# Performance work log

Hardware: AMD Instinct MI355X
Metric: run time of the kernel (lower is better)

## Reference

```python
import jax, jax.numpy as jnp
import numpy as np

N, E, F_IN, H, C = 20000, 320000, 256, 4, 64
D = H * C  # hidden_dim = 256
NEG_SLOPE = 0.2
LN_EPS = 1e-5


def setup_inputs() -> dict:
    key = jax.random.key(0)
    ks = jax.random.split(key, 12)
    x = jax.random.normal(ks[0], (N, F_IN), dtype=jnp.float32)
    # edges guaranteed self-loop-free (PyG GATConv removes then re-adds self loops)
    dst = jax.random.randint(ks[1], (E,), 0, N)
    off = jax.random.randint(ks[2], (E,), 1, N)
    src = (dst + off) % N
    edge_index = jnp.stack([src, dst]).astype(jnp.int64)

    def lin(k, fan_in, shape):
        return jax.random.normal(k, shape, dtype=jnp.float32) / np.sqrt(fan_in)

    W1 = lin(ks[3], F_IN, (F_IN, D)); b1 = jnp.zeros((D,), jnp.float32)
    a_src1 = lin(ks[4], C, (H, C)); a_dst1 = lin(ks[5], C, (H, C))
    W2 = lin(ks[6], D, (D, D)); b2 = jnp.zeros((D,), jnp.float32)
    a_src2 = lin(ks[7], C, (H, C)); a_dst2 = lin(ks[8], C, (H, C))
    g1 = jnp.ones((D,), jnp.float32); be1 = jnp.zeros((D,), jnp.float32)
    g2 = jnp.ones((D,), jnp.float32); be2 = jnp.zeros((D,), jnp.float32)
    attn_w = lin(ks[9], D, (D, 1)); attn_b = jnp.zeros((1,), jnp.float32)
    return dict(x=x, edge_index=edge_index, W1=W1, b1=b1, a_src1=a_src1,
                a_dst1=a_dst1, W2=W2, b2=b2, a_src2=a_src2, a_dst2=a_dst2,
                g1=g1, be1=be1, g2=g2, be2=be2, attn_w=attn_w, attn_b=attn_b)


def _gat_conv(x, src, dst, W, b, a_src, a_dst):
    # x: [N, F] -> h: [N, H, C]
    h = (x @ W).reshape(N, H, C)
    alpha_s = jnp.einsum('nhc,hc->nh', h, a_src)  # [N, H]
    alpha_d = jnp.einsum('nhc,hc->nh', h, a_dst)
    e = jax.nn.leaky_relu(alpha_s[src] + alpha_d[dst], NEG_SLOPE)  # [E', H]
    # segment softmax over edges sharing a destination
    m = jax.ops.segment_max(e, dst, num_segments=N)
    w = jnp.exp(e - m[dst])
    z = jax.ops.segment_sum(w, dst, num_segments=N)
    alpha = w / (z[dst] + 1e-16)
    out = jax.ops.segment_sum(h[src] * alpha[:, :, None], dst, num_segments=N)
    return out.reshape(N, D) + b


def _layernorm(x, g, b):
    mu = x.mean(-1, keepdims=True)
    var = ((x - mu) ** 2).mean(-1, keepdims=True)
    return (x - mu) * jax.lax.rsqrt(var + LN_EPS) * g + b


def reference(x, edge_index, W1, b1, a_src1, a_dst1, W2, b2, a_src2, a_dst2,
              g1, be1, g2, be2, attn_w, attn_b):
    loops = jnp.arange(N, dtype=edge_index.dtype)
    src = jnp.concatenate([edge_index[0], loops])
    dst = jnp.concatenate([edge_index[1], loops])
    x1 = _gat_conv(x, src, dst, W1, b1, a_src1, a_dst1)
    x1 = jax.nn.elu(_layernorm(x1, g1, be1))
    x2 = _gat_conv(x1, src, dst, W2, b2, a_src2, a_dst2)
    x2 = jax.nn.elu(_layernorm(x2, g2, be2) + x1)
    attn = jax.nn.softmax(x2 @ attn_w + attn_b, axis=0)  # softmax over nodes
    pooled = (x2 * attn).sum(axis=0)  # [D]
    return pooled
```

## Files before the change

### kernel.cpp

```cpp
#include <hip/hip_runtime.h>
#include <math.h>

#define N_NODES 20000
#define E_EDGES 320000
#define TOT_E   (E_EDGES + N_NODES)
#define DHID    256
#define NHEAD   4
#define SCAN_NB ((N_NODES + 255) / 256)
#define SPART   32
#define ECAP    128

typedef float f32x4 __attribute__((ext_vector_type(4)));
typedef short short8 __attribute__((ext_vector_type(8)));
typedef unsigned short ushort;

__device__ __forceinline__ float wave_sum(float v) {
#pragma unroll
  for (int off = 32; off; off >>= 1) v += __shfl_xor(v, off);
  return v;
}
__device__ __forceinline__ ushort f2bf(float f) {
  unsigned u = __float_as_uint(f);
  u += 0x7fffu + ((u >> 16) & 1u);
  return (ushort)(u >> 16);
}
__device__ __forceinline__ float bflo(unsigned u) {
  return __uint_as_float(u << 16);
}
__device__ __forceinline__ float bfhi(unsigned u) {
  return __uint_as_float(u & 0xffff0000u);
}

__global__ void hist_kernel(const int* __restrict__ ei, int* __restrict__ deg) {
  int e = blockIdx.x * blockDim.x + threadIdx.x;
  if (e >= TOT_E) return;
  int dst = (e < E_EDGES) ? ei[E_EDGES + e] : (e - E_EDGES);
  atomicAdd(&deg[dst], 1);
}

__global__ __launch_bounds__(256)
void scan_blocks_kernel(const int* __restrict__ deg, int* __restrict__ bsum) {
  __shared__ int ws[4];
  const int t = threadIdx.x;
  const int i = blockIdx.x * 256 + t;
  int v = (i < N_NODES) ? deg[i] : 0;
  int s = v;
#pragma unroll
  for (int off = 32; off; off >>= 1) s += __shfl_xor(s, off);
  if ((t & 63) == 0) ws[t >> 6] = s;
  __syncthreads();
  if (t == 0) bsum[blockIdx.x] = ws[0] + ws[1] + ws[2] + ws[3];
}

__global__ __launch_bounds__(128)
void scan_tops_kernel(const int* __restrict__ bsum, int* __restrict__ boff) {
  __shared__ int tmp[SCAN_NB];
  const int t = threadIdx.x;
  if (t < SCAN_NB) tmp[t] = bsum[t];
  __syncthreads();
  if (t == 0) {
    int run = 0;
    for (int i = 0; i < SCAN_NB; ++i) { int x = tmp[i]; tmp[i] = run; run += x; }
  }
  __syncthreads();
  if (t < SCAN_NB) boff[t] = tmp[t];
}

__global__ __launch_bounds__(256)
void scan_apply_kernel(const int* __restrict__ deg, const int* __restrict__ boff,
                       int* __restrict__ rowp, int* __restrict__ cur) {
  __shared__ int ws[4];
  const int t = threadIdx.x;
  const int lane = t & 63, w = t >> 6;
  const int i = blockIdx.x * 256 + t;
  int v = (i < N_NODES) ? deg[i] : 0;
  int inc = v;
#pragma unroll
  for (int off = 1; off < 64; off <<= 1) {
    int u = __shfl_up(inc, off);
    if (lane >= off) inc += u;
  }
  if (lane == 63) ws[w] = inc;
  __syncthreads();
  int add = boff[blockIdx.x];
#pragma unroll
  for (int k = 0; k < 4; ++k)
    if (k < w) add += ws[k];
  int exc = add + inc - v;
  if (i < N_NODES) {
    rowp[i] = exc;
    cur[i] = exc;
    if (i == N_NODES - 1) rowp[N_NODES] = exc + v;
  }
}

__global__ void scatter_kernel(const int* __restrict__ ei, int* __restrict__ cur,
                               int* __restrict__ colb) {
  int e = blockIdx.x * blockDim.x + threadIdx.x;
  if (e >= TOT_E) return;
  int src, dst;
  if (e < E_EDGES) { src = ei[e]; dst = ei[E_EDGES + e]; }
  else             { src = dst = e - E_EDGES; }
  int pos = atomicAdd(&cur[dst], 1);
  colb[pos] = src;
}

__global__ __launch_bounds__(256)
void conv_inputs_kernel(const float* __restrict__ W1, const float* __restrict__ W2,
                        const float* __restrict__ x, ushort* __restrict__ Wt1,
                        ushort* __restrict__ Wt2, ushort* __restrict__ xb,
                        int* __restrict__ deg) {
  const int b = blockIdx.x;
  if (b < 512) {
    const float* W = (b < 256) ? W1 : W2;
    ushort* Wt = (b < 256) ? Wt1 : Wt2;
    const int n = b & 255;
    const int k = threadIdx.x;
    Wt[n * 256 + k] = f2bf(W[k * 256 + n]);
  } else if (b < 512 + N_NODES * 256 / 8 / 256) {
    int idx = (b - 512) * 256 + threadIdx.x;
    size_t base = (size_t)idx * 8;
    float4 a = *reinterpret_cast<const float4*>(x + base);
    float4 c = *reinterpret_cast<const float4*>(x + base + 4);
    short8 o;
    o[0] = f2bf(a.x); o[1] = f2bf(a.y); o[2] = f2bf(a.z); o[3] = f2bf(a.w);
    o[4] = f2bf(c.x); o[5] = f2bf(c.y); o[6] = f2bf(c.z); o[7] = f2bf(c.w);
    *reinterpret_cast<short8*>(xb + base) = o;
  } else {
    int idx = (b - (512 + N_NODES * 256 / 8 / 256)) * 256 + threadIdx.x;
    if (idx < N_NODES) deg[idx] = 0;
  }
}

__global__ __launch_bounds__(256)
void gemm_alpha_kernel(const ushort* __restrict__ Ab, const ushort* __restrict__ Wt,
                       const float* __restrict__ asrc, const float* __restrict__ adst,
                       ushort* __restrict__ hout, float* __restrict__ as_,
                       float* __restrict__ ad_) {
  __shared__ ushort hs[32 * 256];

  const int t = threadIdx.x;
  const int w = t >> 6;
  const int l = t & 63;
  const int row0 = blockIdx.x * 32;

  const ushort* abase = Ab + (size_t)(row0 + (l & 15)) * 256 + ((l >> 4) * 8);
  const ushort* bbase = Wt + (size_t)(w * 64 + (l & 15)) * 256 + ((l >> 4) * 8);

  f32x4 acc[2][4];
#pragma unroll
  for (int i = 0; i < 2; ++i)
#pragma unroll
    for (int j = 0; j < 4; ++j) acc[i][j] = (f32x4){0.f, 0.f, 0.f, 0.f};

  short8 a0 = *reinterpret_cast<const short8*>(abase);
  short8 a1 = *reinterpret_cast<const short8*>(abase + 16 * 256);
  short8 b0 = *reinterpret_cast<const short8*>(bbase);
  short8 b1 = *reinterpret_cast<const short8*>(bbase + 16 * 256);
  short8 b2 = *reinterpret_cast<const short8*>(bbase + 32 * 256);
  short8 b3 = *reinterpret_cast<const short8*>(bbase + 48 * 256);
#pragma unroll
  for (int kk = 0; kk < 256; kk += 32) {
    short8 na0, na1, nb0, nb1, nb2, nb3;
    if (kk + 32 < 256) {
      na0 = *reinterpret_cast<const short8*>(abase + kk + 32);
      na1 = *reinterpret_cast<const short8*>(abase + 16 * 256 + kk + 32);
      nb0 = *reinterpret_cast<const short8*>(bbase + kk + 32);
      nb1 = *reinterpret_cast<const short8*>(bbase + 16 * 256 + kk + 32);
      nb2 = *reinterpret_cast<const short8*>(bbase + 32 * 256 + kk + 32);
      nb3 = *reinterpret_cast<const short8*>(bbase + 48 * 256 + kk + 32);
    }
    acc[0][0] = __builtin_amdgcn_mfma_f32_16x16x32_bf16(a0, b0, acc[0][0], 0, 0, 0);
    acc[0][1] = __builtin_amdgcn_mfma_f32_16x16x32_bf16(a0, b1, acc[0][1], 0, 0, 0);
    acc[0][2] = __builtin_amdgcn_mfma_f32_16x16x32_bf16(a0, b2, acc[0][2], 0, 0, 0);
    acc[0][3] = __builtin_amdgcn_mfma_f32_16x16x32_bf16(a0, b3, acc[0][3], 0, 0, 0);
    acc[1][0] = __builtin_amdgcn_mfma_f32_16x16x32_bf16(a1, b0, acc[1][0], 0, 0, 0);
    acc[1][1] = __builtin_amdgcn_mfma_f32_16x16x32_bf16(a1, b1, acc[1][1], 0, 0, 0);
    acc[1][2] = __builtin_amdgcn_mfma_f32_16x16x32_bf16(a1, b2, acc[1][2], 0, 0, 0);
    acc[1][3] = __builtin_amdgcn_mfma_f32_16x16x32_bf16(a1, b3, acc[1][3], 0, 0, 0);
    if (kk + 32 < 256) {
      a0 = na0; a1 = na1; b0 = nb0; b1 = nb1; b2 = nb2; b3 = nb3;
    }
  }

  float asj[4], adj[4];
#pragma unroll
  for (int j = 0; j < 4; ++j) {
    asj[j] = asrc[w * 64 + j * 16 + (l & 15)];
    adj[j] = adst[w * 64 + j * 16 + (l & 15)];
  }
#pragma unroll
  for (int i = 0; i < 2; ++i) {
#pragma unroll
    for (int q = 0; q < 4; ++q) {
      float ps = 0.f, pd = 0.f;
#pragma unroll
      for (int j = 0; j < 4; ++j) {
        ps += acc[i][j][q] * asj[j];
        pd += acc[i][j][q] * adj[j];
      }
#pragma unroll
      for (int off = 1; off < 16; off <<= 1) {
        ps += __shfl_xor(ps, off);
        pd += __shfl_xor(pd, off);
      }
      int row = row0 + i * 16 + (l >> 4) * 4 + q;
      if ((l & 15) == 0) {
        as_[row * 4 + w] = ps;
        ad_[row * 4 + w] = pd;
      }
    }
  }

#pragma unroll
  for (int i = 0; i < 2; ++i)
#pragma unroll
    for (int j = 0; j < 4; ++j)
#pragma unroll
      for (int q = 0; q < 4; ++q) {
        int row = i * 16 + (l >> 4) * 4 + q;
        int col = w * 64 + j * 16 + (l & 15);
        hs[row * 256 + col] = f2bf(acc[i][j][q]);
      }
  __syncthreads();
#pragma unroll
  for (int g = 0; g < 4; ++g) {
    int gi = g * 256 + t;
    int row = gi >> 5;
    int slot = gi & 31;
    *reinterpret_cast<short8*>(hout + (size_t)(row0 + row) * 256 + slot * 8) =
        *reinterpret_cast<const short8*>(&hs[row * 256 + slot * 8]);
  }
}

__global__ __launch_bounds__(256)
void attn_gather_ln_kernel(const ushort* __restrict__ h, const float* __restrict__ as_,
                           const float* __restrict__ ad_, const int* __restrict__ rowp,
                           const int* __restrict__ colb, const float* __restrict__ bias,
                           const float* __restrict__ gamma, const float* __restrict__ beta,
                           const ushort* __restrict__ residb, ushort* __restrict__ outb,
                           const float* __restrict__ aw, const float* __restrict__ ab,
                           float* __restrict__ score) {
  __shared__ float ew[4][ECAP][NHEAD];
  __shared__ int   sidx[4][ECAP];

  const int t = threadIdx.x;
  const int wd = t >> 6;
  const int d = blockIdx.x * 4 + wd;
  const int l = t & 63;
  const int start = rowp[d];
  const int deg = rowp[d + 1] - start;
  const int* cb = colb + start;

  const int e16 = l >> 2, hh = l & 3;
  const float adv = ad_[d * 4 + hh];
  const int gh = l >> 4;
  const int c0 = l * 4;
  const ushort* hrow = h + c0;

  float zpart = 0.f;
  float a0 = 0.f, a1 = 0.f, a2 = 0.f, a3 = 0.f;

  for (int base = 0; base < deg; base += ECAP) {
    const int cnt = min(deg - base, ECAP);
    for (int i = e16; i < cnt; i += 16) {
      int s = cb[base + i];
      if (hh == 0) sidx[wd][i] = s;
      float e = as_[s * 4 + hh] + adv;
      e = (e >= 0.f) ? e : 0.2f * e;
      e = fminf(e, 60.f);
      float wv = __expf(e);
      ew[wd][i][hh] = wv;
      zpart += wv;
    }
    int i = 0;
    for (; i + 8 <= cnt; i += 8) {
      int ss[8]; float ww[8]; uint2 hv[8];
#pragma unroll
      for (int k = 0; k < 8; ++k) { ss[k] = sidx[wd][i + k]; ww[k] = ew[wd][i + k][gh]; }
#pragma unroll
      for (int k = 0; k < 8; ++k)
        hv[k] = *reinterpret_cast<const uint2*>(hrow + (size_t)ss[k] * 256);
#pragma unroll
      for (int k = 0; k < 8; ++k) {
        a0 += ww[k] * bflo(hv[k].x); a1 += ww[k] * bfhi(hv[k].x);
        a2 += ww[k] * bflo(hv[k].y); a3 += ww[k] * bfhi(hv[k].y);
      }
    }
    for (; i + 4 <= cnt; i += 4) {
      int ss[4]; float ww[4]; uint2 hv[4];
#pragma unroll
      for (int k = 0; k < 4; ++k) { ss[k] = sidx[wd][i + k]; ww[k] = ew[wd][i + k][gh]; }
#pragma unroll
      for (int k = 0; k < 4; ++k)
        hv[k] = *reinterpret_cast<const uint2*>(hrow + (size_t)ss[k] * 256);
#pragma unroll
      for (int k = 0; k < 4; ++k) {
        a0 += ww[k] * bflo(hv[k].x); a1 += ww[k] * bfhi(hv[k].x);
        a2 += ww[k] * bflo(hv[k].y); a3 += ww[k] * bfhi(hv[k].y);
      }
    }
    for (; i < cnt; ++i) {
      int s = sidx[wd][i];
      float wv = ew[wd][i][gh];
      uint2 hv = *reinterpret_cast<const uint2*>(hrow + (size_t)s * 256);
      a0 += wv * bflo(hv.x);
      a1 += wv * bfhi(hv.x);
      a2 += wv * bflo(hv.y);
      a3 += wv * bfhi(hv.y);
    }
  }

#pragma unroll
  for (int off = 4; off < 64; off <<= 1) zpart += __shfl_xor(zpart, off);
  const float zi = 1.f / (__shfl(zpart, gh) + 1e-16f);

  float4 bi = *reinterpret_cast<const float4*>(bias + c0);
  float v0 = a0 * zi + bi.x, v1 = a1 * zi + bi.y;
  float v2 = a2 * zi + bi.z, v3 = a3 * zi + bi.w;

  float s1 = wave_sum(v0 + v1 + v2 + v3);
  float s2 = wave_sum(v0 * v0 + v1 * v1 + v2 * v2 + v3 * v3);
  float mu = s1 * (1.f / 256.f);
  float var = s2 * (1.f / 256.f) - mu * mu;
  float rstd = rsqrtf(var + 1e-5f);
  float4 ga = *reinterpret_cast<const float4*>(gamma + c0);
  float4 be = *reinterpret_cast<const float4*>(beta + c0);
  float y0 = (v0 - mu) * rstd * ga.x + be.x;
  float y1 = (v1 - mu) * rstd * ga.y + be.y;
  float y2 = (v2 - mu) * rstd * ga.z + be.z;
  float y3 = (v3 - mu) * rstd * ga.w + be.w;
  if (residb) {
    uint2 rv = *reinterpret_cast<const uint2*>(residb + (size_t)d * 256 + c0);
    y0 += bflo(rv.x); y1 += bfhi(rv.x); y2 += bflo(rv.y); y3 += bfhi(rv.y);
  }
  y0 = (y0 > 0.f) ? y0 : expm1f(y0);
  y1 = (y1 > 0.f) ? y1 : expm1f(y1);
  y2 = (y2 > 0.f) ? y2 : expm1f(y2);
  y3 = (y3 > 0.f) ? y3 : expm1f(y3);

  uint2 o;
  o.x = ((unsigned)f2bf(y0)) | (((unsigned)f2bf(y1)) << 16);
  o.y = ((unsigned)f2bf(y2)) | (((unsigned)f2bf(y3)) << 16);
  *reinterpret_cast<uint2*>(outb + (size_t)d * 256 + c0) = o;

  if (score) {
    float4 aww = *reinterpret_cast<const float4*>(aw + c0);
    float sp = wave_sum(y0 * aww.x + y1 * aww.y + y2 * aww.z + y3 * aww.w);
    if (l == 0) score[d] = sp + ab[0];
  }
}

__global__ __launch_bounds__(256)
void score_part_kernel(const float* __restrict__ s, float* __restrict__ pm,
                       float* __restrict__ pz) {
  __shared__ float red[4];
  const int t = threadIdx.x, b = blockIdx.x;
  const int lane = t & 63, wid = t >> 6;
  float m = -INFINITY;
  for (int n = b * 256 + t; n < N_NODES; n += SPART * 256) m = fmaxf(m, s[n]);
#pragma unroll
  for (int off = 32; off; off >>= 1) m = fmaxf(m, __shfl_xor(m, off));
  if (lane == 0) red[wid] = m;
  __syncthreads();
  m = fmaxf(fmaxf(red[0], red[1]), fmaxf(red[2], red[3]));
  __syncthreads();
  float z = 0.f;
  for (int n = b * 256 + t; n < N_NODES; n += SPART * 256) z += __expf(s[n] - m);
  z = wave_sum(z);
  if (lane == 0) red[wid] = z;
  __syncthreads();
  if (t == 0) { pm[b] = m; pz[b] = red[0] + red[1] + red[2] + red[3]; }
}

__global__ __launch_bounds__(64)
void score_comb_kernel(const float* __restrict__ pm, const float* __restrict__ pz,
                       float* __restrict__ mz) {
  const int l = threadIdx.x;
  float m = (l < SPART) ? pm[l] : -INFINITY;
#pragma unroll
  for (int off = 32; off; off >>= 1) m = fmaxf(m, __shfl_xor(m, off));
  float z = (l < SPART) ? pz[l] * __expf(pm[l] - m) : 0.f;
  z = wave_sum(z);
  if (l == 0) { mz[0] = m; mz[1] = z; }
}

__global__ __launch_bounds__(256)
void pool_partial_kernel(const ushort* __restrict__ hb2, const float* __restrict__ s,
                         const float* __restrict__ mz, float* __restrict__ part) {
  __shared__ float red4[4][256];
  const int t = threadIdx.x, b = blockIdx.x;
  const int c4 = t & 63, rsub = t >> 6;
  const float m = mz[0];
  const float invz = 1.f / mz[1];
  f32x4 acc = (f32x4){0.f, 0.f, 0.f, 0.f};
  for (int n = b * 4 + rsub; n < N_NODES; n += 1024) {
    float w = __expf(s[n] - m);
    uint2 hv = *reinterpret_cast<const uint2*>(hb2 + (size_t)n * 256 + c4 * 4);
    acc[0] += w * bflo(hv.x);
    acc[1] += w * bfhi(hv.x);
    acc[2] += w * bflo(hv.y);
    acc[3] += w * bfhi(hv.y);
  }
#pragma unroll
  for (int k = 0; k < 4; ++k) red4[rsub][c4 * 4 + k] = acc[k];
  __syncthreads();
  if (t < 256) {
    float v = red4[0][t] + red4[1][t] + red4[2][t] + red4[3][t];
    part[b * 256 + t] = v * invz;
  }
}

__global__ __launch_bounds__(256)
void pool_final_kernel(const float* __restrict__ part, float* __restrict__ out) {
  const int t = threadIdx.x;
  float acc = 0.f;
  for (int b = 0; b < 256; ++b) acc += part[b * 256 + t];
  out[t] = acc;
}

extern "C" void kernel_launch(void* const* d_in, const int* in_sizes, int n_in,
                              void* d_out, int out_size, void* d_ws, size_t ws_size,
                              hipStream_t stream) {
  const float* x      = (const float*)d_in[0];
  const int*   ei     = (const int*)d_in[1];
  const float* W1     = (const float*)d_in[2];
  const float* b1     = (const float*)d_in[3];
  const float* a_src1 = (const float*)d_in[4];
  const float* a_dst1 = (const float*)d_in[5];
  const float* W2     = (const float*)d_in[6];
  const float* b2     = (const float*)d_in[7];
  const float* a_src2 = (const float*)d_in[8];
  const float* a_dst2 = (const float*)d_in[9];
  const float* g1     = (const float*)d_in[10];
  const float* be1    = (const float*)d_in[11];
  const float* g2     = (const float*)d_in[12];
  const float* be2    = (const float*)d_in[13];
  const float* attn_w = (const float*)d_in[14];
  const float* attn_b = (const float*)d_in[15];
  float* out = (float*)d_out;

  char* p = (char*)d_ws;
  auto alloc = [&](size_t bytes) {
    char* r = p;
    p += (bytes + 255) & ~size_t(255);
    return r;
  };
  ushort* h   = (ushort*)alloc((size_t)N_NODES * 256 * 2);
  ushort* xb  = (ushort*)alloc((size_t)N_NODES * 256 * 2);
  ushort* xb1 = (ushort*)alloc((size_t)N_NODES * 256 * 2);
  ushort* hb2 = (ushort*)alloc((size_t)N_NODES * 256 * 2);
  float* as_  = (float*)alloc((size_t)N_NODES * 4 * 4);
  float* ad_  = (float*)alloc((size_t)N_NODES * 4 * 4);
  float* sbuf = (float*)alloc((size_t)N_NODES * 4);
  float* mz   = (float*)alloc(256);
  float* pm   = (float*)alloc((size_t)SPART * 4);
  float* pz   = (float*)alloc((size_t)SPART * 4);
  float* part = (float*)alloc((size_t)256 * 256 * 4);
  ushort* wt1 = (ushort*)alloc((size_t)256 * 256 * 2);
  ushort* wt2 = (ushort*)alloc((size_t)256 * 256 * 2);
  int* deg    = (int*)alloc((size_t)N_NODES * 4);
  int* rowp   = (int*)alloc((size_t)(N_NODES + 1) * 4);
  int* cur    = (int*)alloc((size_t)N_NODES * 4);
  int* colb   = (int*)alloc((size_t)TOT_E * 4);
  int* bsum   = (int*)alloc((size_t)SCAN_NB * 4);
  int* boff   = (int*)alloc((size_t)SCAN_NB * 4);

  const int EB = (TOT_E + 255) / 256;
  const int GB = N_NODES / 32;
  const int DB = N_NODES / 4;
  const int XB = N_NODES * 256 / 8 / 256;
  const int CONVB = 512 + XB + SCAN_NB;

  conv_inputs_kernel<<<CONVB, 256, 0, stream>>>(W1, W2, x, wt1, wt2, xb, deg);
  hist_kernel<<<EB, 256, 0, stream>>>(ei, deg);
  scan_blocks_kernel<<<SCAN_NB, 256, 0, stream>>>(deg, bsum);
  scan_tops_kernel<<<1, 128, 0, stream>>>(bsum, boff);
  scan_apply_kernel<<<SCAN_NB, 256, 0, stream>>>(deg, boff, rowp, cur);
  scatter_kernel<<<EB, 256, 0, stream>>>(ei, cur, colb);

  gemm_alpha_kernel<<<GB, 256, 0, stream>>>(xb, wt1, a_src1, a_dst1, h, as_, ad_);
  attn_gather_ln_kernel<<<DB, 256, 0, stream>>>(h, as_, ad_, rowp, colb, b1, g1, be1,
                                                nullptr, xb1, nullptr, nullptr, nullptr);
  gemm_alpha_kernel<<<GB, 256, 0, stream>>>(xb1, wt2, a_src2, a_dst2, h, as_, ad_);
  attn_gather_ln_kernel<<<DB, 256, 0, stream>>>(h, as_, ad_, rowp, colb, b2, g2, be2,
                                                xb1, hb2, attn_w, attn_b, sbuf);
  score_part_kernel<<<SPART, 256, 0, stream>>>(sbuf, pm, pz);
  score_comb_kernel<<<1, 64, 0, stream>>>(pm, pz, mz);
  pool_partial_kernel<<<256, 256, 0, stream>>>(hb2, sbuf, mz, part);
  pool_final_kernel<<<1, 256, 0, stream>>>(part, out);
}
```

Baseline: 173.1 us.

## Cut launch count: single-block scan, merge scatter with GEMM, online-softmax pooling

Three launches for the degree prefix scan become one 1024-thread block that handles 20 elements per thread. The edge scatter and the first GEMM+alpha now run as a single launch with block-index dispatch, since neither depends on the other. The attention pooling uses an online softmax inside pool_partial, with the max and sum merged in pool_final, which removes the two score-reduction kernels. The aim is to reduce launch and serialization overhead, at the cost of a serial single-block scan and extra exp work in the pooling loop.

```diff
diff --git a/kernel.cpp b/kernel.cpp
--- a/kernel.cpp
+++ b/kernel.cpp
@@ -6,9 +6,9 @@
 #define TOT_E   (E_EDGES + N_NODES)
 #define DHID    256
 #define NHEAD   4
-#define SCAN_NB ((N_NODES + 255) / 256)
-#define SPART   32
 #define ECAP    128
+#define EB_K    ((TOT_E + 255) / 256)
+#define GB_K    (N_NODES / 32)
 
 typedef float f32x4 __attribute__((ext_vector_type(4)));
 typedef short short8 __attribute__((ext_vector_type(8)));
@@ -38,71 +38,45 @@
   atomicAdd(&deg[dst], 1);
 }
 
-__global__ __launch_bounds__(256)
-void scan_blocks_kernel(const int* __restrict__ deg, int* __restrict__ bsum) {
-  __shared__ int ws[4];
-  const int t = threadIdx.x;
-  const int i = blockIdx.x * 256 + t;
-  int v = (i < N_NODES) ? deg[i] : 0;
-  int s = v;
-#pragma unroll
-  for (int off = 32; off; off >>= 1) s += __shfl_xor(s, off);
-  if ((t & 63) == 0) ws[t >> 6] = s;
-  __syncthreads();
-  if (t == 0) bsum[blockIdx.x] = ws[0] + ws[1] + ws[2] + ws[3];
-}
-
-__global__ __launch_bounds__(128)
-void scan_tops_kernel(const int* __restrict__ bsum, int* __restrict__ boff) {
-  __shared__ int tmp[SCAN_NB];
-  const int t = threadIdx.x;
-  if (t < SCAN_NB) tmp[t] = bsum[t];
-  __syncthreads();
-  if (t == 0) {
-    int run = 0;
-    for (int i = 0; i < SCAN_NB; ++i) { int x = tmp[i]; tmp[i] = run; run += x; }
-  }
-  __syncthreads();
-  if (t < SCAN_NB) boff[t] = tmp[t];
-}
-
-__global__ __launch_bounds__(256)
-void scan_apply_kernel(const int* __restrict__ deg, const int* __restrict__ boff,
-                       int* __restrict__ rowp, int* __restrict__ cur) {
-  __shared__ int ws[4];
+__global__ __launch_bounds__(1024)
+void scan_kernel(const int* __restrict__ deg, int* __restrict__ rowp,
+                 int* __restrict__ cur) {
+  __shared__ int wsum[16];
   const int t = threadIdx.x;
   const int lane = t & 63, w = t >> 6;
-  const int i = blockIdx.x * 256 + t;
-  int v = (i < N_NODES) ? deg[i] : 0;
-  int inc = v;
+  const int base = t * 20;
+  int vals[20];
+  int sum = 0;
+#pragma unroll
+  for (int k = 0; k < 20; ++k) {
+    int i = base + k;
+    int v = (i < N_NODES) ? deg[i] : 0;
+    vals[k] = v;
+    sum += v;
+  }
+  int inc = sum;
 #pragma unroll
   for (int off = 1; off < 64; off <<= 1) {
     int u = __shfl_up(inc, off);
     if (lane >= off) inc += u;
   }
-  if (lane == 63) ws[w] = inc;
-  __syncthreads();
-  int add = boff[blockIdx.x];
-#pragma unroll
-  for (int k = 0; k < 4; ++k)
-    if (k < w) add += ws[k];
-  int exc = add + inc - v;
-  if (i < N_NODES) {
-    rowp[i] = exc;
-    cur[i] = exc;
-    if (i == N_NODES - 1) rowp[N_NODES] = exc + v;
-  }
-}
-
-__global__ void scatter_kernel(const int* __restrict__ ei, int* __restrict__ cur,
-                               int* __restrict__ colb) {
-  int e = blockIdx.x * blockDim.x + threadIdx.x;
-  if (e >= TOT_E) return;
-  int src, dst;
-  if (e < E_EDGES) { src = ei[e]; dst = ei[E_EDGES + e]; }
-  else             { src = dst = e - E_EDGES; }
-  int pos = atomicAdd(&cur[dst], 1);
-  colb[pos] = src;
+  if (lane == 63) wsum[w] = inc;
+  __syncthreads();
+  int add = 0;
+#pragma unroll
+  for (int k = 0; k < 16; ++k)
+    if (k < w) add += wsum[k];
+  int run = add + inc - sum;
+#pragma unroll
+  for (int k = 0; k < 20; ++k) {
+    int i = base + k;
+    if (i < N_NODES) {
+      rowp[i] = run;
+      cur[i] = run;
+      run += vals[k];
+    }
+  }
+  if (t == 0) rowp[N_NODES] = TOT_E;
 }
 
 __global__ __launch_bounds__(256)
@@ -133,6 +107,120 @@
 }
 
 __global__ __launch_bounds__(256)
+void scatter_gemm_kernel(const int* __restrict__ ei, int* __restrict__ cur,
+                         int* __restrict__ colb, const ushort* __restrict__ Ab,
+                         const ushort* __restrict__ Wt, const float* __restrict__ asrc,
+                         const float* __restrict__ adst, ushort* __restrict__ hout,
+                         float* __restrict__ as_, float* __restrict__ ad_) {
+  __shared__ ushort hs[32 * 256];
+
+  if (blockIdx.x < EB_K) {
+    int e = blockIdx.x * 256 + threadIdx.x;
+    if (e < TOT_E) {
+      int src, dst;
+      if (e < E_EDGES) { src = ei[e]; dst = ei[E_EDGES + e]; }
+      else             { src = dst = e - E_EDGES; }
+      int pos = atomicAdd(&cur[dst], 1);
+      colb[pos] = src;
+    }
+    return;
+  }
+
+  const int t = threadIdx.x;
+  const int w = t >> 6;
+  const int l = t & 63;
+  const int row0 = (blockIdx.x - EB_K) * 32;
+
+  const ushort* abase = Ab + (size_t)(row0 + (l & 15)) * 256 + ((l >> 4) * 8);
+  const ushort* bbase = Wt + (size_t)(w * 64 + (l & 15)) * 256 + ((l >> 4) * 8);
+
+  f32x4 acc[2][4];
+#pragma unroll
+  for (int i = 0; i < 2; ++i)
+#pragma unroll
+    for (int j = 0; j < 4; ++j) acc[i][j] = (f32x4){0.f, 0.f, 0.f, 0.f};
+
+  short8 a0 = *reinterpret_cast<const short8*>(abase);
+  short8 a1 = *reinterpret_cast<const short8*>(abase + 16 * 256);
+  short8 b0 = *reinterpret_cast<const short8*>(bbase);
+  short8 b1 = *reinterpret_cast<const short8*>(bbase + 16 * 256);
+  short8 b2 = *reinterpret_cast<const short8*>(bbase + 32 * 256);
+  short8 b3 = *reinterpret_cast<const short8*>(bbase + 48 * 256);
+#pragma unroll
+  for (int kk = 0; kk < 256; kk += 32) {
+    short8 na0, na1, nb0, nb1, nb2, nb3;
+    if (kk + 32 < 256) {
+      na0 = *reinterpret_cast<const short8*>(abase + kk + 32);
+      na1 = *reinterpret_cast<const short8*>(abase + 16 * 256 + kk + 32);
+      nb0 = *reinterpret_cast<const short8*>(bbase + kk + 32);
+      nb1 = *reinterpret_cast<const short8*>(bbase + 16 * 256 + kk + 32);
+      nb2 = *reinterpret_cast<const short8*>(bbase + 32 * 256 + kk + 32);
+      nb3 = *reinterpret_cast<const short8*>(bbase + 48 * 256 + kk + 32);
+    }
+    acc[0][0] = __builtin_amdgcn_mfma_f32_16x16x32_bf16(a0, b0, acc[0][0], 0, 0, 0);
+    acc[0][1] = __builtin_amdgcn_mfma_f32_16x16x32_bf16(a0, b1, acc[0][1], 0, 0, 0);
+    acc[0][2] = __builtin_amdgcn_mfma_f32_16x16x32_bf16(a0, b2, acc[0][2], 0, 0, 0);
+    acc[0][3] = __builtin_amdgcn_mfma_f32_16x16x32_bf16(a0, b3, acc[0][3], 0, 0, 0);
+    acc[1][0] = __builtin_amdgcn_mfma_f32_16x16x32_bf16(a1, b0, acc[1][0], 0, 0, 0);
+    acc[1][1] = __builtin_amdgcn_mfma_f32_16x16x32_bf16(a1, b1, acc[1][1], 0, 0, 0);
+    acc[1][2] = __builtin_amdgcn_mfma_f32_16x16x32_bf16(a1, b2, acc[1][2], 0, 0, 0);
+    acc[1][3] = __builtin_amdgcn_mfma_f32_16x16x32_bf16(a1, b3, acc[1][3], 0, 0, 0);
+    if (kk + 32 < 256) {
+      a0 = na0; a1 = na1; b0 = nb0; b1 = nb1; b2 = nb2; b3 = nb3;
+    }
+  }
+
+  float asj[4], adj[4];
+#pragma unroll
+  for (int j = 0; j < 4; ++j) {
+    asj[j] = asrc[w * 64 + j * 16 + (l & 15)];
+    adj[j] = adst[w * 64 + j * 16 + (l & 15)];
+  }
+#pragma unroll
+  for (int i = 0; i < 2; ++i) {
+#pragma unroll
+    for (int q = 0; q < 4; ++q) {
+      float ps = 0.f, pd = 0.f;
+#pragma unroll
+      for (int j = 0; j < 4; ++j) {
+        ps += acc[i][j][q] * asj[j];
+        pd += acc[i][j][q] * adj[j];
+      }
+#pragma unroll
+      for (int off = 1; off < 16; off <<= 1) {
+        ps += __shfl_xor(ps, off);
+        pd += __shfl_xor(pd, off);
+      }
+      int row = row0 + i * 16 + (l >> 4) * 4 + q;
+      if ((l & 15) == 0) {
+        as_[row * 4 + w] = ps;
+        ad_[row * 4 + w] = pd;
+      }
+    }
+  }
+
+#pragma unroll
+  for (int i = 0; i < 2; ++i)
+#pragma unroll
+    for (int j = 0; j < 4; ++j)
+#pragma unroll
+      for (int q = 0; q < 4; ++q) {
+        int row = i * 16 + (l >> 4) * 4 + q;
+        int col = w * 64 + j * 16 + (l & 15);
+        hs[row * 256 + col] = f2bf(acc[i][j][q]);
+      }
+  __syncthreads();
+#pragma unroll
+  for (int g = 0; g < 4; ++g) {
+    int gi = g * 256 + t;
+    int row = gi >> 5;
+    int slot = gi & 31;
+    *reinterpret_cast<short8*>(hout + (size_t)(row0 + row) * 256 + slot * 8) =
+        *reinterpret_cast<const short8*>(&hs[row * 256 + slot * 8]);
+  }
+}
+
+__global__ __launch_bounds__(256)
 void gemm_alpha_kernel(const ushort* __restrict__ Ab, const ushort* __restrict__ Wt,
                        const float* __restrict__ asrc, const float* __restrict__ adst,
                        ushort* __restrict__ hout, float* __restrict__ as_,
@@ -352,71 +440,67 @@
 }
 
 __global__ __launch_bounds__(256)
-void score_part_kernel(const float* __restrict__ s, float* __restrict__ pm,
-                       float* __restrict__ pz) {
-  __shared__ float red[4];
-  const int t = threadIdx.x, b = blockIdx.x;
-  const int lane = t & 63, wid = t >> 6;
-  float m = -INFINITY;
-  for (int n = b * 256 + t; n < N_NODES; n += SPART * 256) m = fmaxf(m, s[n]);
-#pragma unroll
-  for (int off = 32; off; off >>= 1) m = fmaxf(m, __shfl_xor(m, off));
-  if (lane == 0) red[wid] = m;
-  __syncthreads();
-  m = fmaxf(fmaxf(red[0], red[1]), fmaxf(red[2], red[3]));
-  __syncthreads();
-  float z = 0.f;
-  for (int n = b * 256 + t; n < N_NODES; n += SPART * 256) z += __expf(s[n] - m);
-  z = wave_sum(z);
-  if (lane == 0) red[wid] = z;
-  __syncthreads();
-  if (t == 0) { pm[b] = m; pz[b] = red[0] + red[1] + red[2] + red[3]; }
-}
-
-__global__ __launch_bounds__(64)
-void score_comb_kernel(const float* __restrict__ pm, const float* __restrict__ pz,
-                       float* __restrict__ mz) {
-  const int l = threadIdx.x;
-  float m = (l < SPART) ? pm[l] : -INFINITY;
-#pragma unroll
-  for (int off = 32; off; off >>= 1) m = fmaxf(m, __shfl_xor(m, off));
-  float z = (l < SPART) ? pz[l] * __expf(pm[l] - m) : 0.f;
-  z = wave_sum(z);
-  if (l == 0) { mz[0] = m; mz[1] = z; }
-}
-
-__global__ __launch_bounds__(256)
 void pool_partial_kernel(const ushort* __restrict__ hb2, const float* __restrict__ s,
-                         const float* __restrict__ mz, float* __restrict__ part) {
+                         float* __restrict__ part, float* __restrict__ pm,
+                         float* __restrict__ pz) {
   __shared__ float red4[4][256];
+  __shared__ float mzs[4][2];
   const int t = threadIdx.x, b = blockIdx.x;
   const int c4 = t & 63, rsub = t >> 6;
-  const float m = mz[0];
-  const float invz = 1.f / mz[1];
+  float m = -INFINITY, z = 0.f;
   f32x4 acc = (f32x4){0.f, 0.f, 0.f, 0.f};
   for (int n = b * 4 + rsub; n < N_NODES; n += 1024) {
-    float w = __expf(s[n] - m);
+    float sv = s[n];
+    float mn = fmaxf(m, sv);
+    float f = __expf(m - mn);
+    float w = __expf(sv - mn);
+    z = z * f + w;
     uint2 hv = *reinterpret_cast<const uint2*>(hb2 + (size_t)n * 256 + c4 * 4);
-    acc[0] += w * bflo(hv.x);
-    acc[1] += w * bfhi(hv.x);
-    acc[2] += w * bflo(hv.y);
-    acc[3] += w * bfhi(hv.y);
+    acc[0] = acc[0] * f + w * bflo(hv.x);
+    acc[1] = acc[1] * f + w * bfhi(hv.x);
+    acc[2] = acc[2] * f + w * bflo(hv.y);
+    acc[3] = acc[3] * f + w * bfhi(hv.y);
+    m = mn;
   }
 #pragma unroll
   for (int k = 0; k < 4; ++k) red4[rsub][c4 * 4 + k] = acc[k];
-  __syncthreads();
-  if (t < 256) {
-    float v = red4[0][t] + red4[1][t] + red4[2][t] + red4[3][t];
-    part[b * 256 + t] = v * invz;
+  if (c4 == 0) { mzs[rsub][0] = m; mzs[rsub][1] = z; }
+  __syncthreads();
+  float M = fmaxf(fmaxf(mzs[0][0], mzs[1][0]), fmaxf(mzs[2][0], mzs[3][0]));
+  float e0 = __expf(mzs[0][0] - M), e1 = __expf(mzs[1][0] - M);
+  float e2 = __expf(mzs[2][0] - M), e3 = __expf(mzs[3][0] - M);
+  float v = red4[0][t] * e0 + red4[1][t] * e1 + red4[2][t] * e2 + red4[3][t] * e3;
+  part[b * 256 + t] = v;
+  if (t == 0) {
+    pm[b] = M;
+    pz[b] = mzs[0][1] * e0 + mzs[1][1] * e1 + mzs[2][1] * e2 + mzs[3][1] * e3;
   }
 }
 
 __global__ __launch_bounds__(256)
-void pool_final_kernel(const float* __restrict__ part, float* __restrict__ out) {
-  const int t = threadIdx.x;
+void pool_final_kernel(const float* __restrict__ part, const float* __restrict__ pm,
+                       const float* __restrict__ pz, float* __restrict__ out) {
+  __shared__ float lm[256], le[256], red[4];
+  const int t = threadIdx.x, lane = t & 63, wid = t >> 6;
+  lm[t] = pm[t];
+  __syncthreads();
+  float M = lm[t];
+#pragma unroll
+  for (int off = 32; off; off >>= 1) M = fmaxf(M, __shfl_xor(M, off));
+  if (lane == 0) red[wid] = M;
+  __syncthreads();
+  M = fmaxf(fmaxf(red[0], red[1]), fmaxf(red[2], red[3]));
+  __syncthreads();
+  float e = __expf(lm[t] - M);
+  le[t] = e;
+  float zc = pz[t] * e;
+  zc = wave_sum(zc);
+  if (lane == 0) red[wid] = zc;
+  __syncthreads();
+  float Z = red[0] + red[1] + red[2] + red[3];
   float acc = 0.f;
-  for (int b = 0; b < 256; ++b) acc += part[b * 256 + t];
-  out[t] = acc;
+  for (int b = 0; b < 256; ++b) acc += part[b * 256 + t] * le[b];
+  out[t] = acc / Z;
 }
 
 extern "C" void kernel_launch(void* const* d_in, const int* in_sizes, int n_in,
@@ -453,9 +537,8 @@
   float* as_  = (float*)alloc((size_t)N_NODES * 4 * 4);
   float* ad_  = (float*)alloc((size_t)N_NODES * 4 * 4);
   float* sbuf = (float*)alloc((size_t)N_NODES * 4);
-  float* mz   = (float*)alloc(256);
-  float* pm   = (float*)alloc((size_t)SPART * 4);
-  float* pz   = (float*)alloc((size_t)SPART * 4);
+  float* pm   = (float*)alloc((size_t)256 * 4);
+  float* pz   = (float*)alloc((size_t)256 * 4);
   float* part = (float*)alloc((size_t)256 * 256 * 4);
   ushort* wt1 = (ushort*)alloc((size_t)256 * 256 * 2);
   ushort* wt2 = (ushort*)alloc((size_t)256 * 256 * 2);
@@ -463,30 +546,22 @@
   int* rowp   = (int*)alloc((size_t)(N_NODES + 1) * 4);
   int* cur    = (int*)alloc((size_t)N_NODES * 4);
   int* colb   = (int*)alloc((size_t)TOT_E * 4);
-  int* bsum   = (int*)alloc((size_t)SCAN_NB * 4);
-  int* boff   = (int*)alloc((size_t)SCAN_NB * 4);
-
-  const int EB = (TOT_E + 255) / 256;
-  const int GB = N_NODES / 32;
+
   const int DB = N_NODES / 4;
   const int XB = N_NODES * 256 / 8 / 256;
+  const int SCAN_NB = (N_NODES + 255) / 256;
   const int CONVB = 512 + XB + SCAN_NB;
 
   conv_inputs_kernel<<<CONVB, 256, 0, stream>>>(W1, W2, x, wt1, wt2, xb, deg);
-  hist_kernel<<<EB, 256, 0, stream>>>(ei, deg);
-  scan_blocks_kernel<<<SCAN_NB, 256, 0, stream>>>(deg, bsum);
-  scan_tops_kernel<<<1, 128, 0, stream>>>(bsum, boff);
-  scan_apply_kernel<<<SCAN_NB, 256, 0, stream>>>(deg, boff, rowp, cur);
-  scatter_kernel<<<EB, 256, 0, stream>>>(ei, cur, colb);
-
-  gemm_alpha_kernel<<<GB, 256, 0, stream>>>(xb, wt1, a_src1, a_dst1, h, as_, ad_);
+  hist_kernel<<<EB_K, 256, 0, stream>>>(ei, deg);
+  scan_kernel<<<1, 1024, 0, stream>>>(deg, rowp, cur);
+  scatter_gemm_kernel<<<EB_K + GB_K, 256, 0, stream>>>(
+      ei, cur, colb, xb, wt1, a_src1, a_dst1, h, as_, ad_);
   attn_gather_ln_kernel<<<DB, 256, 0, stream>>>(h, as_, ad_, rowp, colb, b1, g1, be1,
                                                 nullptr, xb1, nullptr, nullptr, nullptr);
-  gemm_alpha_kernel<<<GB, 256, 0, stream>>>(xb1, wt2, a_src2, a_dst2, h, as_, ad_);
+  gemm_alpha_kernel<<<GB_K, 256, 0, stream>>>(xb1, wt2, a_src2, a_dst2, h, as_, ad_);
   attn_gather_ln_kernel<<<DB, 256, 0, stream>>>(h, as_, ad_, rowp, colb, b2, g2, be2,
                                                 xb1, hb2, attn_w, attn_b, sbuf);
-  score_part_kernel<<<SPART, 256, 0, stream>>>(sbuf, pm, pz);
-  score_comb_kernel<<<1, 64, 0, stream>>>(pm, pz, mz);
-  pool_partial_kernel<<<256, 256, 0, stream>>>(hb2, sbuf, mz, part);
-  pool_final_kernel<<<1, 256, 0, stream>>>(part, out);
-}
+  pool_partial_kernel<<<256, 256, 0, stream>>>(hb2, sbuf, part, pm, pz);
+  pool_final_kernel<<<1, 256, 0, stream>>>(part, pm, pz, out);
+}
```

After: 183.2 us. 5.8% more time.
